# Optimization experiments

Hardware: AMD Instinct MI355X
Metric: run time of the kernel (lower is better)

Reference implementation:

```python
import jax, jax.numpy as jnp
import numpy as np

N_HEAD, D_MODEL, D_HEAD = 16, 1024, 64
SEQ, BATCH = 1024, 8
SCALE = 1.0 / (D_HEAD ** 0.5)
LN_EPS = 1e-5


def setup_inputs() -> dict:
    key = jax.random.key(0)
    ks = jax.random.split(key, 16)
    dk = N_HEAD * D_HEAD  # == D_MODEL
    init_qkv = 1.0 / np.sqrt(D_MODEL)
    init_out = 1.0 / np.sqrt(dk)
    u = lambda k, shp, lo, hi: jax.random.uniform(k, shp, jnp.float32, lo, hi)
    inp = {
        'dec_inp': jax.random.normal(ks[0], (SEQ, BATCH, D_MODEL), jnp.float32),
        'attn_mask': jnp.triu(jnp.ones((SEQ, SEQ), dtype=bool), k=1),  # causal
        'query_mean': u(ks[1], (dk, D_MODEL), -init_qkv, init_qkv),
        'key_mean': u(ks[2], (dk, D_MODEL), -init_qkv, init_qkv),
        'value_mean': u(ks[3], (dk, D_MODEL), -init_qkv, init_qkv),
        'query_std': u(ks[4], (dk, D_MODEL), 2 * np.log(init_qkv), np.log(init_qkv)),
        'key_std': u(ks[5], (dk, D_MODEL), 2 * np.log(init_qkv), np.log(init_qkv)),
        'value_std': u(ks[6], (dk, D_MODEL), 2 * np.log(init_qkv), np.log(init_qkv)),
        'output_mean': u(ks[7], (D_MODEL, dk), -init_out, init_out),
        'output_std': u(ks[8], (D_MODEL, dk), 2 * np.log(init_out), np.log(init_out)),
        'ln_gamma': jnp.ones((D_MODEL,), jnp.float32),
        'ln_beta': jnp.zeros((D_MODEL,), jnp.float32),
        # per-forward reparameterization noise (training mode)
        'eps_q': jax.random.normal(ks[9], (dk, D_MODEL), jnp.float32),
        'eps_k': jax.random.normal(ks[10], (dk, D_MODEL), jnp.float32),
        'eps_v': jax.random.normal(ks[11], (dk, D_MODEL), jnp.float32),
        'eps_o': jax.random.normal(ks[12], (D_MODEL, dk), jnp.float32),
    }
    return inp


def _forward(dec_inp, query_mean, key_mean, value_mean, query_std, key_std,
             value_std, output_mean, output_std, ln_gamma, ln_beta,
             eps_q, eps_k, eps_v, eps_o, attn_mask):
    S, B, _ = dec_inp.shape
    # Bayesian weight sampling: w = mean + eps * exp(std)
    qw = query_mean + eps_q * jnp.exp(query_std)
    kw = key_mean + eps_k * jnp.exp(key_std)
    vw = value_mean + eps_v * jnp.exp(value_std)
    # NOTE: original code (bug kept for faithfulness) builds the output weight
    # from value_mean + output_diff, not output_mean.
    ow = value_mean + eps_o * jnp.exp(output_std)

    head_q = (dec_inp @ qw.T).reshape(S, B, N_HEAD, D_HEAD)
    head_k = (dec_inp @ kw.T).reshape(S, B, N_HEAD, D_HEAD)
    head_v = (dec_inp @ vw.T).reshape(S, B, N_HEAD, D_HEAD)

    score = jnp.einsum('ibnd,jbnd->ijbn', head_q, head_k) * SCALE
    score = jnp.where(attn_mask[:, :, None, None], -jnp.inf, score)
    prob = jax.nn.softmax(score, axis=1)  # softmax over j (key) axis
    attn_vec = jnp.einsum('ijbn,jbnd->ibnd', prob, head_v).reshape(S, B, N_HEAD * D_HEAD)

    attn_out = attn_vec @ ow.T
    x = dec_inp + attn_out
    mu = jnp.mean(x, axis=-1, keepdims=True)
    var = jnp.var(x, axis=-1, keepdims=True)
    output = (x - mu) * jax.lax.rsqrt(var + LN_EPS) * ln_gamma + ln_beta

    theta_mean = jnp.concatenate([query_mean, key_mean, value_mean, output_mean.T], -1)
    theta_std = jnp.concatenate([query_std, key_std, value_std, output_std.T], -1)
    kl = jnp.mean(theta_mean ** 2 - theta_std * 2.0 + jnp.exp(theta_std * 2.0)) / 2.0
    return output, kl


def reference(dec_inp, attn_mask, query_mean, key_mean, value_mean, query_std,
              key_std, value_std, output_mean, output_std, ln_gamma, ln_beta,
              eps_q, eps_k, eps_v, eps_o):
    return _forward(dec_inp, query_mean, key_mean, value_mean, query_std,
                    key_std, value_std, output_mean, output_std, ln_gamma,
                    ln_beta, eps_q, eps_k, eps_v, eps_o, attn_mask)
```

## Files before the change

### kernel.cpp

```cpp
#include <hip/hip_runtime.h>

typedef _Float16 f16x8 __attribute__((ext_vector_type(8)));
typedef _Float16 f16x4 __attribute__((ext_vector_type(4)));
typedef float    f32x4 __attribute__((ext_vector_type(4)));

static __device__ __forceinline__ f32x4 mfma16(f16x8 a, f16x8 b, f32x4 c) {
    return __builtin_amdgcn_mfma_f32_16x16x32_f16(a, b, c, 0, 0, 0);
}

static __device__ __forceinline__ void gload_lds16(const _Float16* g, _Float16* lds) {
    __builtin_amdgcn_global_load_lds(
        (const __attribute__((address_space(1))) unsigned int*)g,
        (__attribute__((address_space(3))) unsigned int*)lds, 16, 0, 0);
}

__global__ __launch_bounds__(256) void k_prep(
    const float* __restrict__ qm, const float* __restrict__ km, const float* __restrict__ vm,
    const float* __restrict__ qs, const float* __restrict__ ks, const float* __restrict__ vs,
    const float* __restrict__ om, const float* __restrict__ os,
    const float* __restrict__ eq, const float* __restrict__ ek,
    const float* __restrict__ ev, const float* __restrict__ eo,
    _Float16* __restrict__ wq, _Float16* __restrict__ wk,
    _Float16* __restrict__ wv, _Float16* __restrict__ wo,
    float* __restrict__ part,
    const float* __restrict__ dec, _Float16* __restrict__ xh)
{
    if (blockIdx.x >= 4096) {
        int i = ((blockIdx.x - 4096) * 256 + threadIdx.x) * 4;
        float4 v = *(const float4*)&dec[i];
        f16x4 hv;
        hv[0] = (_Float16)v.x; hv[1] = (_Float16)v.y;
        hv[2] = (_Float16)v.z; hv[3] = (_Float16)v.w;
        *(f16x4*)&xh[i] = hv;
        return;
    }
    int i = blockIdx.x * 256 + threadIdx.x;
    float aqm = qm[i], akm = km[i], avm = vm[i];
    float aqs = qs[i], aks = ks[i], avs = vs[i];
    float aom = om[i], aos = os[i];
    wq[i] = (_Float16)(aqm + eq[i] * __expf(aqs));
    wk[i] = (_Float16)(akm + ek[i] * __expf(aks));
    wv[i] = (_Float16)(avm + ev[i] * __expf(avs));
    wo[i] = (_Float16)(avm + eo[i] * __expf(aos));
    float t = aqm*aqm - 2.f*aqs + __expf(2.f*aqs)
            + akm*akm - 2.f*aks + __expf(2.f*aks)
            + avm*avm - 2.f*avs + __expf(2.f*avs)
            + aom*aom - 2.f*aos + __expf(2.f*aos);
    #pragma unroll
    for (int m = 1; m < 64; m <<= 1) t += __shfl_xor(t, m, 64);
    __shared__ float red[4];
    int w = threadIdx.x >> 6, lane = threadIdx.x & 63;
    if (lane == 0) red[w] = t;
    __syncthreads();
    if (threadIdx.x == 0) part[blockIdx.x] = red[0] + red[1] + red[2] + red[3];
}

__global__ __launch_bounds__(256) void k_gemm(
    const _Float16* __restrict__ A, const _Float16* __restrict__ B0,
    _Float16* __restrict__ C0, const float* __restrict__ resid,
    float* __restrict__ xout, int mode)
{
    __shared__ __align__(16) _Float16 As[128 * 64];
    __shared__ __align__(16) _Float16 Bs[128 * 64];
    const int K = 1024, N = 1024;
    const _Float16* Bp = B0 + (size_t)blockIdx.z * 1048576u;
    _Float16* Cp = C0 + (size_t)blockIdx.z * 8388608u;
    int flat = blockIdx.y * 8 + blockIdx.x;
    int xcd = flat & 7, j = flat >> 3;
    int tM = (xcd * 8 + (j & 7)) * 128;
    int tN = (j >> 3) * 128;
    int tid = threadIdx.x, w = tid >> 6, lane = tid & 63;
    int wm = w & 1, wn = w >> 1;
    int q = lane >> 4, r = lane & 15;
    int csrc = ((lane & 7) ^ (lane >> 3)) * 8;
    int srow = lane >> 3;
    f32x4 acc[4][4] = {};
    for (int kk = 0; kk < K; kk += 64) {
        __syncthreads();
        #pragma unroll
        for (int i = 0; i < 4; ++i) {
            int chunk = w * 4 + i;
            int row = chunk * 8 + srow;
            gload_lds16(A  + (size_t)(tM + row) * K + kk + csrc, &As[chunk * 512]);
            gload_lds16(Bp + (size_t)(tN + row) * K + kk + csrc, &Bs[chunk * 512]);
        }
        __syncthreads();
        #pragma unroll
        for (int kc = 0; kc < 2; ++kc) {
            f16x8 af[4], bf[4];
            #pragma unroll
            for (int m = 0; m < 4; ++m) {
                int row = wm*64 + m*16 + r;
                int pos = ((kc*4 + q) ^ (r & 7)) * 8;
                af[m] = *(const f16x8*)&As[row*64 + pos];
            }
            #pragma unroll
            for (int n = 0; n < 4; ++n) {
                int row = wn*64 + n*16 + r;
                int pos = ((kc*4 + q) ^ (r & 7)) * 8;
                bf[n] = *(const f16x8*)&Bs[row*64 + pos];
            }
            #pragma unroll
            for (int m = 0; m < 4; ++m)
                #pragma unroll
                for (int n = 0; n < 4; ++n)
                    acc[m][n] = mfma16(af[m], bf[n], acc[m][n]);
        }
    }
    float sc = (mode == 0 && blockIdx.z == 0) ? 0.125f : 1.0f;
    #pragma unroll
    for (int m = 0; m < 4; ++m)
      #pragma unroll
      for (int n = 0; n < 4; ++n)
        #pragma unroll
        for (int t = 0; t < 4; ++t) {
            int row = tM + wm*64 + m*16 + q*4 + t;
            int col = tN + wn*64 + n*16 + r;
            size_t o = (size_t)row * N + col;
            if (mode == 0) Cp[o] = (_Float16)(acc[m][n][t] * sc);
            else           xout[o] = resid[o] + acc[m][n][t];
        }
}

__global__ __launch_bounds__(256) void k_vtrans(const _Float16* __restrict__ V,
                                                _Float16* __restrict__ Vt)
{
    __shared__ __align__(16) _Float16 L[64 * 72];
    int c = blockIdx.x;
    int b = c >> 4, h = c & 15;
    int s0 = blockIdx.y * 64;
    int tid = threadIdx.x;
    #pragma unroll
    for (int rep = 0; rep < 2; ++rep) {
        int idx = rep * 256 + tid;
        int sl = idx >> 3, ch = idx & 7;
        f16x8 v = *(const f16x8*)&V[((size_t)(s0 + sl) * 8 + b) * 1024 + h * 64 + ch * 8];
        *(f16x8*)&L[sl * 72 + ch * 8] = v;
    }
    __syncthreads();
    #pragma unroll
    for (int rep = 0; rep < 2; ++rep) {
        int idx = rep * 256 + tid;
        int d = idx >> 3, c2 = idx & 7;
        f16x8 o;
        #pragma unroll
        for (int e = 0; e < 8; ++e) o[e] = L[(c2 * 8 + e) * 72 + d];
        *(f16x8*)&Vt[((size_t)c * 64 + d) * 1024 + s0 + c2 * 8] = o;
    }
}

__global__ __launch_bounds__(256, 4) void k_attn(
    const _Float16* __restrict__ Qb, const _Float16* __restrict__ Kb,
    const _Float16* __restrict__ Vtg, _Float16* __restrict__ AVo)
{
    __shared__ __align__(16) _Float16 Ks[64 * 64];
    __shared__ __align__(16) _Float16 Vs[64 * 64];
    __shared__ __align__(16) _Float16 Ps[4 * 32 * 72];
    const int bh = blockIdx.x;
    const int b = bh & 7, h = bh >> 3;
    const int cbh = b * 16 + h;
    const int qt = blockIdx.y;
    const int tid = threadIdx.x, w = tid >> 6, lane = tid & 63;
    const int q = lane >> 4, r = lane & 15;
    const int i0 = qt * 128 + w * 32;
    const int csrc = ((lane & 7) ^ (lane >> 3)) * 8;
    const int srow = lane >> 3;

    f16x8 qf[2][2];
    #pragma unroll
    for (int it = 0; it < 2; ++it)
      #pragma unroll
      for (int kc = 0; kc < 2; ++kc)
        qf[it][kc] = *(const f16x8*)&Qb[((size_t)(i0 + it*16 + r)*8 + b)*1024 + h*64 + kc*32 + q*8];

    f32x4 ot[4][2] = {};
    float mrun[2] = {-1e30f, -1e30f}, lrun[2] = {0.f, 0.f};
    _Float16* Pw = &Ps[w * 2304];

    auto tile = [&](int kt, bool MASK) __attribute__((always_inline)) {
        __syncthreads();
        #pragma unroll
        for (int ii = 0; ii < 2; ++ii) {
            int chunk = w * 2 + ii;
            int row = chunk * 8 + srow;
            gload_lds16(Kb  + ((size_t)(kt*64 + row)*8 + b)*1024 + h*64 + csrc, &Ks[chunk*512]);
            gload_lds16(Vtg + ((size_t)(cbh*64 + row))*1024 + kt*64 + csrc,     &Vs[chunk*512]);
        }
        __syncthreads();

        f32x4 st[4][2] = {};
        #pragma unroll
        for (int kc = 0; kc < 2; ++kc) {
            f16x8 kf[4];
            #pragma unroll
            for (int jt = 0; jt < 4; ++jt) {
                int pos = ((kc*4 + q) ^ (r & 7)) * 8;
                kf[jt] = *(const f16x8*)&Ks[(jt*16 + r)*64 + pos];
            }
            #pragma unroll
            for (int jt = 0; jt < 4; ++jt)
              #pragma unroll
              for (int it = 0; it < 2; ++it)
                st[jt][it] = mfma16(kf[jt], qf[it][kc], st[jt][it]);
        }

        #pragma unroll
        for (int it = 0; it < 2; ++it) {
            if (MASK) {
                int il = i0 + it*16 + r;
                #pragma unroll
                for (int jt = 0; jt < 4; ++jt)
                  #pragma unroll
                  for (int t = 0; t < 4; ++t)
                    if (kt*64 + jt*16 + q*4 + t > il) st[jt][it][t] = -1e30f;
            }
            float mx = -1e30f;
            #pragma unroll
            for (int jt = 0; jt < 4; ++jt) {
                f32x4 s4 = st[jt][it];
                mx = fmaxf(mx, fmaxf(fmaxf(s4[0], s4[1]), fmaxf(s4[2], s4[3])));
            }
            mx = fmaxf(mx, __shfl_xor(mx, 16, 64));
            mx = fmaxf(mx, __shfl_xor(mx, 32, 64));
            float mnew = fmaxf(mrun[it], mx);
            float al = __expf(mrun[it] - mnew);
            mrun[it] = mnew;
            float ps = 0.f;
            #pragma unroll
            for (int jt = 0; jt < 4; ++jt) {
                f16x4 hv;
                #pragma unroll
                for (int t = 0; t < 4; ++t) {
                    float e = __expf(st[jt][it][t] - mnew);
                    ps += e;
                    hv[t] = (_Float16)e;
                }
                *(f16x4*)&Pw[(it*16 + r)*72 + jt*16 + q*4] = hv;
            }
            ps += __shfl_xor(ps, 16, 64);
            ps += __shfl_xor(ps, 32, 64);
            lrun[it] = lrun[it] * al + ps;
            #pragma unroll
            for (int dtb = 0; dtb < 4; ++dtb) ot[dtb][it] *= al;
        }

        #pragma unroll
        for (int kc = 0; kc < 2; ++kc) {
            f16x8 vf[4], pf[2];
            #pragma unroll
            for (int dtb = 0; dtb < 4; ++dtb) {
                int pos = ((kc*4 + q) ^ (r & 7)) * 8;
                vf[dtb] = *(const f16x8*)&Vs[(dtb*16 + r)*64 + pos];
            }
            #pragma unroll
            for (int it = 0; it < 2; ++it)
                pf[it] = *(const f16x8*)&Pw[(it*16 + r)*72 + kc*32 + q*8];
            #pragma unroll
            for (int dtb = 0; dtb < 4; ++dtb)
              #pragma unroll
              for (int it = 0; it < 2; ++it)
                ot[dtb][it] = mfma16(vf[dtb], pf[it], ot[dtb][it]);
        }
    };

    for (int kt = 0; kt < 2*qt; ++kt) tile(kt, false);
    tile(2*qt,     true);
    tile(2*qt + 1, true);

    #pragma unroll
    for (int it = 0; it < 2; ++it) {
        float inv = 1.f / lrun[it];
        int s = i0 + it*16 + r;
        #pragma unroll
        for (int dtb = 0; dtb < 4; ++dtb) {
            f16x4 hv;
            #pragma unroll
            for (int t = 0; t < 4; ++t) hv[t] = (_Float16)(ot[dtb][it][t] * inv);
            *(f16x4*)&AVo[((size_t)s*8 + b)*1024 + h*64 + dtb*16 + q*4] = hv;
        }
    }
}

__global__ __launch_bounds__(256) void k_ln(float* __restrict__ x,
    const float* __restrict__ g, const float* __restrict__ bta,
    const float* __restrict__ part)
{
    __shared__ float rs[4], rs2[4];
    int w = threadIdx.x >> 6, lane = threadIdx.x & 63;
    if (blockIdx.x == 8192) {
        float s = 0.f;
        for (int i = threadIdx.x; i < 4096; i += 256) s += part[i];
        #pragma unroll
        for (int m = 1; m < 64; m <<= 1) s += __shfl_xor(s, m, 64);
        if (lane == 0) rs[w] = s;
        __syncthreads();
        if (threadIdx.x == 0)
            x[8388608] = (rs[0] + rs[1] + rs[2] + rs[3]) * (0.5f / 4194304.f);
        return;
    }
    int row = blockIdx.x;
    float* xr = x + (size_t)row * 1024;
    int t4 = threadIdx.x * 4;
    float4 v = *(const float4*)&xr[t4];
    float s  = v.x + v.y + v.z + v.w;
    float s2 = v.x*v.x + v.y*v.y + v.z*v.z + v.w*v.w;
    #pragma unroll
    for (int m = 1; m < 64; m <<= 1) { s += __shfl_xor(s, m, 64); s2 += __shfl_xor(s2, m, 64); }
    if (lane == 0) { rs[w] = s; rs2[w] = s2; }
    __syncthreads();
    s  = rs[0] + rs[1] + rs[2] + rs[3];
    s2 = rs2[0] + rs2[1] + rs2[2] + rs2[3];
    float mu = s * (1.f / 1024.f);
    float var = s2 * (1.f / 1024.f) - mu * mu;
    float rstd = rsqrtf(var + 1e-5f);
    float4 gv = *(const float4*)&g[t4];
    float4 bv = *(const float4*)&bta[t4];
    float4 ov;
    ov.x = (v.x - mu) * rstd * gv.x + bv.x;
    ov.y = (v.y - mu) * rstd * gv.y + bv.y;
    ov.z = (v.z - mu) * rstd * gv.z + bv.z;
    ov.w = (v.w - mu) * rstd * gv.w + bv.w;
    *(float4*)&xr[t4] = ov;
}

extern "C" void kernel_launch(void* const* d_in, const int* in_sizes, int n_in,
                              void* d_out, int out_size, void* d_ws, size_t ws_size,
                              hipStream_t stream)
{
    (void)in_sizes; (void)n_in; (void)out_size; (void)ws_size;
    const float* dec   = (const float*)d_in[0];
    const float* qm    = (const float*)d_in[2];
    const float* km    = (const float*)d_in[3];
    const float* vm    = (const float*)d_in[4];
    const float* qs    = (const float*)d_in[5];
    const float* ks    = (const float*)d_in[6];
    const float* vs    = (const float*)d_in[7];
    const float* om    = (const float*)d_in[8];
    const float* os    = (const float*)d_in[9];
    const float* gamma = (const float*)d_in[10];
    const float* beta  = (const float*)d_in[11];
    const float* eq    = (const float*)d_in[12];
    const float* ek    = (const float*)d_in[13];
    const float* ev    = (const float*)d_in[14];
    const float* eo    = (const float*)d_in[15];

    char* ws = (char*)d_ws;
    _Float16* WQ   = (_Float16*)ws;
    float*    PART = (float*)(ws + (8ull  << 20));
    _Float16* XH   = (_Float16*)(ws + (9ull  << 20));
    _Float16* Qh   = (_Float16*)(ws + (25ull << 20));
    _Float16* Kh   = Qh + 8388608;
    _Float16* Vh   = Qh + 16777216;
    _Float16* Vtg  = XH;
    _Float16* AV   = Vh;
    float*    out  = (float*)d_out;

    k_prep<<<dim3(12288), dim3(256), 0, stream>>>(
        qm, km, vm, qs, ks, vs, om, os, eq, ek, ev, eo,
        WQ, WQ + 1048576, WQ + 2097152, WQ + 3145728, PART, dec, XH);
    k_gemm<<<dim3(8, 64, 3), dim3(256), 0, stream>>>(XH, WQ, Qh, dec, out, 0);
    k_vtrans<<<dim3(128, 16), dim3(256), 0, stream>>>(Vh, Vtg);
    k_attn<<<dim3(128, 8), dim3(256), 0, stream>>>(Qh, Kh, Vtg, AV);
    k_gemm<<<dim3(8, 64, 1), dim3(256), 0, stream>>>(AV, WQ + 3145728, Qh, dec, out, 1);
    k_ln<<<dim3(8193), dim3(256), 0, stream>>>(out, gamma, beta, PART);
}
```

Before: 338.3 us.

## Rewrite GEMM with 256x256 tiles and double-buffered LDS prefetch

Replaces the 128x128 single-buffered GEMM with a 512-thread kernel computing 256x256 tiles. It double-buffers A/B in LDS and issues the next K-slice's global-to-LDS loads while MFMAs run on the current slice, raising MFMA priority with setprio and using explicit barriers. This targets load stalls and low arithmetic intensity per tile. The trade-offs are much more LDS (128KB per block), fewer blocks (384 or 128 in total), and possible tail imbalance on the single output-projection GEMM.

```diff
diff --git a/kernel.cpp b/kernel.cpp
--- a/kernel.cpp
+++ b/kernel.cpp
@@ -55,70 +55,104 @@
     if (threadIdx.x == 0) part[blockIdx.x] = red[0] + red[1] + red[2] + red[3];
 }
 
-__global__ __launch_bounds__(256) void k_gemm(
+__global__ __launch_bounds__(512, 2) void k_gemm3(
     const _Float16* __restrict__ A, const _Float16* __restrict__ B0,
     _Float16* __restrict__ C0, const float* __restrict__ resid,
     float* __restrict__ xout, int mode)
 {
-    __shared__ __align__(16) _Float16 As[128 * 64];
-    __shared__ __align__(16) _Float16 Bs[128 * 64];
+    __shared__ __align__(16) _Float16 As[2][256 * 64];
+    __shared__ __align__(16) _Float16 Bs[2][256 * 64];
     const int K = 1024, N = 1024;
     const _Float16* Bp = B0 + (size_t)blockIdx.z * 1048576u;
     _Float16* Cp = C0 + (size_t)blockIdx.z * 8388608u;
-    int flat = blockIdx.y * 8 + blockIdx.x;
+
+    int flat = blockIdx.y * 4 + blockIdx.x;
     int xcd = flat & 7, j = flat >> 3;
-    int tM = (xcd * 8 + (j & 7)) * 128;
-    int tN = (j >> 3) * 128;
+    int tM = (xcd * 4 + (j & 3)) * 256;
+    int tN = (j >> 2) * 256;
+
     int tid = threadIdx.x, w = tid >> 6, lane = tid & 63;
-    int wm = w & 1, wn = w >> 1;
+    int wm = w >> 2, wn = w & 3;
     int q = lane >> 4, r = lane & 15;
-    int csrc = ((lane & 7) ^ (lane >> 3)) * 8;
     int srow = lane >> 3;
-    f32x4 acc[4][4] = {};
-    for (int kk = 0; kk < K; kk += 64) {
-        __syncthreads();
-        #pragma unroll
-        for (int i = 0; i < 4; ++i) {
-            int chunk = w * 4 + i;
-            int row = chunk * 8 + srow;
-            gload_lds16(A  + (size_t)(tM + row) * K + kk + csrc, &As[chunk * 512]);
-            gload_lds16(Bp + (size_t)(tN + row) * K + kk + csrc, &Bs[chunk * 512]);
-        }
-        __syncthreads();
+    int csrc = ((lane & 7) ^ srow) * 8;
+
+    const _Float16* Ag = A  + (size_t)(tM + w * 32 + srow) * K + csrc;
+    const _Float16* Bg = Bp + (size_t)(tN + w * 32 + srow) * K + csrc;
+
+    f32x4 acc[8][4] = {};
+
+    #pragma unroll
+    for (int jj = 0; jj < 4; ++jj) {
+        gload_lds16(Ag + (size_t)(jj * 8) * K, &As[0][(w * 4 + jj) * 512]);
+        gload_lds16(Bg + (size_t)(jj * 8) * K, &Bs[0][(w * 4 + jj) * 512]);
+    }
+    asm volatile("s_waitcnt vmcnt(0)" ::: "memory");
+    __builtin_amdgcn_s_barrier();
+
+    #pragma unroll 2
+    for (int t = 0; t < 16; ++t) {
+        const int cur = t & 1, nxt = cur ^ 1;
+        const int kn = ((t + 1) & 15) * 64;
         #pragma unroll
         for (int kc = 0; kc < 2; ++kc) {
-            f16x8 af[4], bf[4];
-            #pragma unroll
-            for (int m = 0; m < 4; ++m) {
-                int row = wm*64 + m*16 + r;
-                int pos = ((kc*4 + q) ^ (r & 7)) * 8;
-                af[m] = *(const f16x8*)&As[row*64 + pos];
-            }
-            #pragma unroll
-            for (int n = 0; n < 4; ++n) {
-                int row = wn*64 + n*16 + r;
-                int pos = ((kc*4 + q) ^ (r & 7)) * 8;
-                bf[n] = *(const f16x8*)&Bs[row*64 + pos];
-            }
-            #pragma unroll
-            for (int m = 0; m < 4; ++m)
+            f16x8 bf[4];
+            #pragma unroll
+            for (int mq = 0; mq < 2; ++mq) {
+                int pos = ((kc * 4 + q) ^ (r & 7)) * 8;
+                if (mq == 0) {
+                    #pragma unroll
+                    for (int n = 0; n < 4; ++n)
+                        bf[n] = *(const f16x8*)&Bs[cur][(wn * 64 + n * 16 + r) * 64 + pos];
+                }
+                f16x8 af[4];
                 #pragma unroll
-                for (int n = 0; n < 4; ++n)
-                    acc[m][n] = mfma16(af[m], bf[n], acc[m][n]);
-        }
-    }
+                for (int i = 0; i < 4; ++i)
+                    af[i] = *(const f16x8*)&As[cur][(wm * 128 + (mq * 4 + i) * 16 + r) * 64 + pos];
+                if (kc == 0) {
+                    if (mq == 0) {
+                        #pragma unroll
+                        for (int jj = 0; jj < 4; ++jj)
+                            gload_lds16(Ag + (size_t)(jj * 8) * K + kn,
+                                        &As[nxt][(w * 4 + jj) * 512]);
+                    } else {
+                        #pragma unroll
+                        for (int jj = 0; jj < 4; ++jj)
+                            gload_lds16(Bg + (size_t)(jj * 8) * K + kn,
+                                        &Bs[nxt][(w * 4 + jj) * 512]);
+                    }
+                }
+                __builtin_amdgcn_s_barrier();
+                asm volatile("s_waitcnt lgkmcnt(0)" ::: "memory");
+                __builtin_amdgcn_sched_barrier(0);
+                __builtin_amdgcn_s_setprio(1);
+                #pragma unroll
+                for (int i = 0; i < 4; ++i)
+                    #pragma unroll
+                    for (int n = 0; n < 4; ++n)
+                        acc[mq * 4 + i][n] = mfma16(af[i], bf[n], acc[mq * 4 + i][n]);
+                __builtin_amdgcn_s_setprio(0);
+                __builtin_amdgcn_sched_barrier(0);
+                if (kc == 1 && mq == 1) {
+                    asm volatile("s_waitcnt vmcnt(0)" ::: "memory");
+                }
+                __builtin_amdgcn_s_barrier();
+            }
+        }
+    }
+
     float sc = (mode == 0 && blockIdx.z == 0) ? 0.125f : 1.0f;
     #pragma unroll
-    for (int m = 0; m < 4; ++m)
+    for (int m = 0; m < 8; ++m)
       #pragma unroll
       for (int n = 0; n < 4; ++n)
         #pragma unroll
-        for (int t = 0; t < 4; ++t) {
-            int row = tM + wm*64 + m*16 + q*4 + t;
-            int col = tN + wn*64 + n*16 + r;
+        for (int tt = 0; tt < 4; ++tt) {
+            int row = tM + wm * 128 + m * 16 + q * 4 + tt;
+            int col = tN + wn * 64 + n * 16 + r;
             size_t o = (size_t)row * N + col;
-            if (mode == 0) Cp[o] = (_Float16)(acc[m][n][t] * sc);
-            else           xout[o] = resid[o] + acc[m][n][t];
+            if (mode == 0) Cp[o] = (_Float16)(acc[m][n][tt] * sc);
+            else           xout[o] = resid[o] + acc[m][n][tt];
         }
 }
 
@@ -358,9 +392,9 @@
     k_prep<<<dim3(12288), dim3(256), 0, stream>>>(
         qm, km, vm, qs, ks, vs, om, os, eq, ek, ev, eo,
         WQ, WQ + 1048576, WQ + 2097152, WQ + 3145728, PART, dec, XH);
-    k_gemm<<<dim3(8, 64, 3), dim3(256), 0, stream>>>(XH, WQ, Qh, dec, out, 0);
+    k_gemm3<<<dim3(4, 32, 3), dim3(512), 0, stream>>>(XH, WQ, Qh, dec, out, 0);
     k_vtrans<<<dim3(128, 16), dim3(256), 0, stream>>>(Vh, Vtg);
     k_attn<<<dim3(128, 8), dim3(256), 0, stream>>>(Qh, Kh, Vtg, AV);
-    k_gemm<<<dim3(8, 64, 1), dim3(256), 0, stream>>>(AV, WQ + 3145728, Qh, dec, out, 1);
+    k_gemm3<<<dim3(4, 32, 1), dim3(512), 0, stream>>>(AV, WQ + 3145728, Qh, dec, out, 1);
     k_ln<<<dim3(8193), dim3(256), 0, stream>>>(out, gamma, beta, PART);
 }
```

Result: slower. 369.3 us (+9.2%).

## Double-buffer K/V tiles in attention, reorder query tiles, vectorize weight prep

Applied to the files above, without the earlier changes.

The attention kernel now double-buffers the K and V tiles in LDS. It prefetches the next tile with async global-to-LDS loads while computing the current one, and uses one barrier per iteration instead of two. Query-tile indices are permuted through a lookup constant so that long and short causal workloads are interleaved across the grid. The prep kernel processes four weights per thread with vector loads and stores, which cuts its block count and the number of KL partial sums. The extra LDS lowers the occupancy hint from 4 to 3 blocks per CU.

```diff
diff --git a/kernel.cpp b/kernel.cpp
--- a/kernel.cpp
+++ b/kernel.cpp
@@ -25,8 +25,8 @@
     float* __restrict__ part,
     const float* __restrict__ dec, _Float16* __restrict__ xh)
 {
-    if (blockIdx.x >= 4096) {
-        int i = ((blockIdx.x - 4096) * 256 + threadIdx.x) * 4;
+    if (blockIdx.x >= 1024) {
+        int i = ((blockIdx.x - 1024) * 256 + threadIdx.x) * 4;
         float4 v = *(const float4*)&dec[i];
         f16x4 hv;
         hv[0] = (_Float16)v.x; hv[1] = (_Float16)v.y;
@@ -34,18 +34,29 @@
         *(f16x4*)&xh[i] = hv;
         return;
     }
-    int i = blockIdx.x * 256 + threadIdx.x;
-    float aqm = qm[i], akm = km[i], avm = vm[i];
-    float aqs = qs[i], aks = ks[i], avs = vs[i];
-    float aom = om[i], aos = os[i];
-    wq[i] = (_Float16)(aqm + eq[i] * __expf(aqs));
-    wk[i] = (_Float16)(akm + ek[i] * __expf(aks));
-    wv[i] = (_Float16)(avm + ev[i] * __expf(avs));
-    wo[i] = (_Float16)(avm + eo[i] * __expf(aos));
-    float t = aqm*aqm - 2.f*aqs + __expf(2.f*aqs)
-            + akm*akm - 2.f*aks + __expf(2.f*aks)
-            + avm*avm - 2.f*avs + __expf(2.f*avs)
-            + aom*aom - 2.f*aos + __expf(2.f*aos);
+    int i = (blockIdx.x * 256 + threadIdx.x) * 4;
+    f32x4 aqm = *(const f32x4*)&qm[i], akm = *(const f32x4*)&km[i], avm = *(const f32x4*)&vm[i];
+    f32x4 aqs = *(const f32x4*)&qs[i], aks = *(const f32x4*)&ks[i], avs = *(const f32x4*)&vs[i];
+    f32x4 aom = *(const f32x4*)&om[i], aos = *(const f32x4*)&os[i];
+    f32x4 veq = *(const f32x4*)&eq[i], vek = *(const f32x4*)&ek[i];
+    f32x4 vev = *(const f32x4*)&ev[i], veo = *(const f32x4*)&eo[i];
+    f16x4 hq, hk, hv, ho;
+    float t = 0.f;
+    #pragma unroll
+    for (int j = 0; j < 4; ++j) {
+        hq[j] = (_Float16)(aqm[j] + veq[j] * __expf(aqs[j]));
+        hk[j] = (_Float16)(akm[j] + vek[j] * __expf(aks[j]));
+        hv[j] = (_Float16)(avm[j] + vev[j] * __expf(avs[j]));
+        ho[j] = (_Float16)(avm[j] + veo[j] * __expf(aos[j]));
+        t += aqm[j]*aqm[j] - 2.f*aqs[j] + __expf(2.f*aqs[j])
+           + akm[j]*akm[j] - 2.f*aks[j] + __expf(2.f*aks[j])
+           + avm[j]*avm[j] - 2.f*avs[j] + __expf(2.f*avs[j])
+           + aom[j]*aom[j] - 2.f*aos[j] + __expf(2.f*aos[j]);
+    }
+    *(f16x4*)&wq[i] = hq;
+    *(f16x4*)&wk[i] = hk;
+    *(f16x4*)&wv[i] = hv;
+    *(f16x4*)&wo[i] = ho;
     #pragma unroll
     for (int m = 1; m < 64; m <<= 1) t += __shfl_xor(t, m, 64);
     __shared__ float red[4];
@@ -149,17 +160,17 @@
     }
 }
 
-__global__ __launch_bounds__(256, 4) void k_attn(
+__global__ __launch_bounds__(256, 3) void k_attn(
     const _Float16* __restrict__ Qb, const _Float16* __restrict__ Kb,
     const _Float16* __restrict__ Vtg, _Float16* __restrict__ AVo)
 {
-    __shared__ __align__(16) _Float16 Ks[64 * 64];
-    __shared__ __align__(16) _Float16 Vs[64 * 64];
+    __shared__ __align__(16) _Float16 Ks[2][64 * 64];
+    __shared__ __align__(16) _Float16 Vs[2][64 * 64];
     __shared__ __align__(16) _Float16 Ps[4 * 32 * 72];
     const int bh = blockIdx.x;
     const int b = bh & 7, h = bh >> 3;
     const int cbh = b * 16 + h;
-    const int qt = blockIdx.y;
+    const int qt = (0x15623740u >> (blockIdx.y * 4)) & 7;
     const int tid = threadIdx.x, w = tid >> 6, lane = tid & 63;
     const int q = lane >> 4, r = lane & 15;
     const int i0 = qt * 128 + w * 32;
@@ -177,17 +188,17 @@
     float mrun[2] = {-1e30f, -1e30f}, lrun[2] = {0.f, 0.f};
     _Float16* Pw = &Ps[w * 2304];
 
-    auto tile = [&](int kt, bool MASK) __attribute__((always_inline)) {
-        __syncthreads();
+    auto stage = [&](int kt, int buf) __attribute__((always_inline)) {
         #pragma unroll
         for (int ii = 0; ii < 2; ++ii) {
             int chunk = w * 2 + ii;
             int row = chunk * 8 + srow;
-            gload_lds16(Kb  + ((size_t)(kt*64 + row)*8 + b)*1024 + h*64 + csrc, &Ks[chunk*512]);
-            gload_lds16(Vtg + ((size_t)(cbh*64 + row))*1024 + kt*64 + csrc,     &Vs[chunk*512]);
-        }
-        __syncthreads();
-
+            gload_lds16(Kb  + ((size_t)(kt*64 + row)*8 + b)*1024 + h*64 + csrc, &Ks[buf][chunk*512]);
+            gload_lds16(Vtg + ((size_t)(cbh*64 + row))*1024 + kt*64 + csrc,     &Vs[buf][chunk*512]);
+        }
+    };
+
+    auto tile = [&](int kt, int buf, bool MASK) __attribute__((always_inline)) {
         f32x4 st[4][2] = {};
         #pragma unroll
         for (int kc = 0; kc < 2; ++kc) {
@@ -195,7 +206,7 @@
             #pragma unroll
             for (int jt = 0; jt < 4; ++jt) {
                 int pos = ((kc*4 + q) ^ (r & 7)) * 8;
-                kf[jt] = *(const f16x8*)&Ks[(jt*16 + r)*64 + pos];
+                kf[jt] = *(const f16x8*)&Ks[buf][(jt*16 + r)*64 + pos];
             }
             #pragma unroll
             for (int jt = 0; jt < 4; ++jt)
@@ -250,7 +261,7 @@
             #pragma unroll
             for (int dtb = 0; dtb < 4; ++dtb) {
                 int pos = ((kc*4 + q) ^ (r & 7)) * 8;
-                vf[dtb] = *(const f16x8*)&Vs[(dtb*16 + r)*64 + pos];
+                vf[dtb] = *(const f16x8*)&Vs[buf][(dtb*16 + r)*64 + pos];
             }
             #pragma unroll
             for (int it = 0; it < 2; ++it)
@@ -263,9 +274,20 @@
         }
     };
 
-    for (int kt = 0; kt < 2*qt; ++kt) tile(kt, false);
-    tile(2*qt,     true);
-    tile(2*qt + 1, true);
+    stage(0, 0);
+    __syncthreads();
+    for (int kt = 0; kt < 2*qt; ++kt) {
+        stage(kt + 1, (kt + 1) & 1);
+        tile(kt, kt & 1, false);
+        __syncthreads();
+    }
+    {
+        int kt = 2*qt;
+        stage(kt + 1, (kt + 1) & 1);
+        tile(kt, kt & 1, true);
+        __syncthreads();
+        tile(kt + 1, (kt + 1) & 1, true);
+    }
 
     #pragma unroll
     for (int it = 0; it < 2; ++it) {
@@ -289,7 +311,7 @@
     int w = threadIdx.x >> 6, lane = threadIdx.x & 63;
     if (blockIdx.x == 8192) {
         float s = 0.f;
-        for (int i = threadIdx.x; i < 4096; i += 256) s += part[i];
+        for (int i = threadIdx.x; i < 1024; i += 256) s += part[i];
         #pragma unroll
         for (int m = 1; m < 64; m <<= 1) s += __shfl_xor(s, m, 64);
         if (lane == 0) rs[w] = s;
@@ -355,7 +377,7 @@
     _Float16* AV   = Vh;
     float*    out  = (float*)d_out;
 
-    k_prep<<<dim3(12288), dim3(256), 0, stream>>>(
+    k_prep<<<dim3(9216), dim3(256), 0, stream>>>(
         qm, km, vm, qs, ks, vs, om, os, eq, ek, ev, eo,
         WQ, WQ + 1048576, WQ + 2097152, WQ + 3145728, PART, dec, XH);
     k_gemm<<<dim3(8, 64, 3), dim3(256), 0, stream>>>(XH, WQ, Qh, dec, out, 0);
```

Result: faster. 308.4 us (-8.8%).
